# Optimization experiments

Hardware: AMD Instinct MI355X
Metric: run time of the kernel (lower is better)

## Reference

```python
import jax, jax.numpy as jnp
import numpy as np

N_NODES = 20000
N_EDGES = 320000
F_IN, H1, H2, N_CLS = 128, 512, 256, 40
NEG_SLOPE = 0.2


def _glorot(key, shape):
    lim = float(np.sqrt(6.0 / (shape[0] + shape[-1])))
    return jax.random.uniform(key, shape, jnp.float32, -lim, lim)


def setup_inputs() -> dict:
    key = jax.random.key(0)
    ks = jax.random.split(key, 12)
    x = jax.random.normal(ks[0], (N_NODES, F_IN), jnp.float32)
    edge_index = jax.random.randint(ks[1], (2, N_EDGES), 0, N_NODES, jnp.int64)
    params = {}
    dims = [(F_IN, H1), (H1, H2), (H2, N_CLS)]
    for i, (din, dout) in enumerate(dims, start=1):
        params[f"W{i}"] = _glorot(ks[3 * i - 1], (din, dout))
        params[f"a{i}s"] = _glorot(ks[3 * i], (1, dout))[0]
        params[f"a{i}d"] = _glorot(ks[3 * i + 1], (1, dout))[0]
        params[f"b{i}"] = jnp.zeros((dout,), jnp.float32)
    return {"x": x, "edge_index": edge_index, **params}


def gat_conv(x, src, dst, W, a_src, a_dst, b, num_nodes):
    # PyG GATConv, heads=1: h = xW; e_ij = LeakyReLU(a_src.h_j + a_dst.h_i)
    # alpha = softmax over incoming edges of target i; out_i = sum_j alpha_ij h_j + b
    h = x @ W                                        # [N, Dout]
    alpha_s = h @ a_src                              # [N]
    alpha_d = h @ a_dst                              # [N]
    e = jax.nn.leaky_relu(alpha_s[src] + alpha_d[dst], NEG_SLOPE)  # [E]
    m = jax.ops.segment_max(e, dst, num_segments=num_nodes)        # [N]
    ex = jnp.exp(e - m[dst])
    denom = jax.ops.segment_sum(ex, dst, num_segments=num_nodes)   # [N]
    alpha = ex / denom[dst]
    out = jax.ops.segment_sum(alpha[:, None] * h[src], dst, num_segments=num_nodes)
    return out + b


def reference(x, edge_index, W1, a1s, a1d, b1, W2, a2s, a2d, b2, W3, a3s, a3d, b3):
    n = x.shape[0]
    # PyG GATConv adds self-loops by default
    loops = jnp.arange(n, dtype=edge_index.dtype)
    src = jnp.concatenate([edge_index[0], loops])
    dst = jnp.concatenate([edge_index[1], loops])
    h = jax.nn.relu(gat_conv(x, src, dst, W1, a1s, a1d, b1, n))
    h = jax.nn.relu(gat_conv(h, src, dst, W2, a2s, a2d, b2, n))
    h = gat_conv(h, src, dst, W3, a3s, a3d, b3, n)
    return jax.nn.log_softmax(h, axis=1)
```

## Files before the change

### kernel.cpp

```cpp
#include <hip/hip_runtime.h>
#include <math.h>

#define N_NODES 20000
#define N_EDGESC 320000
#define ET (N_EDGESC + N_NODES)
#define F_IN 128
#define H1 512
#define H2 256
#define N_CLS 40
#define NEG_SLOPE 0.2f

typedef __attribute__((ext_vector_type(8))) short short8;
typedef __attribute__((ext_vector_type(4))) float floatx4;

__device__ __forceinline__ unsigned short f2bf(float x) {
    unsigned u = __float_as_uint(x);
    unsigned r = (u + 0x7fffu + ((u >> 16) & 1u)) >> 16;
    return (unsigned short)r;
}
__device__ __forceinline__ float bflo(unsigned v) { return __uint_as_float(v << 16); }
__device__ __forceinline__ float bfhi(unsigned v) { return __uint_as_float(v & 0xffff0000u); }
__device__ __forceinline__ float leaky(float e) { return (e > 0.f) ? e : e * NEG_SLOPE; }

template <int DIN, bool IN_BF16>
__device__ __forceinline__ void gemv2_body(int node, int lane, const void* __restrict__ in,
                                           const float* __restrict__ wvs,
                                           const float* __restrict__ wvd,
                                           float* __restrict__ als, float* __restrict__ ald) {
    constexpr int C = DIN / 64;
    float ss = 0.f, sd = 0.f;
    if constexpr (IN_BF16) {
        const unsigned short* r = (const unsigned short*)in + (size_t)node * DIN + lane * C;
        float f[C];
        if constexpr (C == 8) {
            uint4 v = *(const uint4*)r;
            f[0] = bflo(v.x); f[1] = bfhi(v.x); f[2] = bflo(v.y); f[3] = bfhi(v.y);
            f[4] = bflo(v.z); f[5] = bfhi(v.z); f[6] = bflo(v.w); f[7] = bfhi(v.w);
        } else {
            uint2 v = *(const uint2*)r;
            f[0] = bflo(v.x); f[1] = bfhi(v.x); f[2] = bflo(v.y); f[3] = bfhi(v.y);
        }
        #pragma unroll
        for (int c = 0; c < C; ++c) {
            ss += f[c] * wvs[lane * C + c];
            sd += f[c] * wvd[lane * C + c];
        }
    } else {
        const float* r = (const float*)in + (size_t)node * DIN + lane * 2;
        float2 v = *(const float2*)r;
        ss = v.x * wvs[lane * 2] + v.y * wvs[lane * 2 + 1];
        sd = v.x * wvd[lane * 2] + v.y * wvd[lane * 2 + 1];
    }
    #pragma unroll
    for (int off = 32; off; off >>= 1) {
        ss += __shfl_xor(ss, off);
        sd += __shfl_xor(sd, off);
    }
    if (lane == 0) { als[node] = ss; ald[node] = sd; }
}

#define NCT (F_IN * H1 + H1 * H2 + H2 * N_CLS)
#define PB_CASTX 2500
#define PB_CASTT ((NCT + 255) / 256)
#define PB_WA 224
#define PB_ZERO ((N_NODES + 255) / 256)

__global__ __launch_bounds__(256) void prep_kernel(
        const float* __restrict__ x, unsigned short* __restrict__ xb,
        const float* __restrict__ W1, unsigned short* __restrict__ w1t,
        const float* __restrict__ a1s, const float* __restrict__ a1d,
        const float* __restrict__ W2, unsigned short* __restrict__ w2t,
        const float* __restrict__ a2s, const float* __restrict__ a2d,
        const float* __restrict__ W3, unsigned short* __restrict__ w3t,
        const float* __restrict__ a3s, const float* __restrict__ a3d,
        float* __restrict__ wab, int* __restrict__ deg) {
    int bid = blockIdx.x, t = threadIdx.x;
    if (bid < PB_CASTX) {
        int i = (bid * 256 + t) * 4;
        float4 v = *(const float4*)(x + i);
        ushort4 o = { f2bf(v.x), f2bf(v.y), f2bf(v.z), f2bf(v.w) };
        *(ushort4*)(xb + i) = o;
    } else if (bid < PB_CASTX + PB_CASTT) {
        int i = (bid - PB_CASTX) * 256 + t;
        if (i < F_IN * H1) {
            int k = i >> 9, n = i & 511;
            w1t[n * F_IN + k] = f2bf(W1[i]);
        } else if (i < F_IN * H1 + H1 * H2) {
            int j = i - F_IN * H1;
            int k = j >> 8, n = j & 255;
            w2t[n * H1 + k] = f2bf(W2[j]);
        } else if (i < NCT) {
            int j = i - (F_IN * H1 + H1 * H2);
            int k = j / N_CLS, n = j - k * N_CLS;
            w3t[n * H2 + k] = f2bf(W3[j]);
        }
    } else if (bid < PB_CASTX + PB_CASTT + PB_WA) {
        int lane = t & 63;
        int row = (bid - PB_CASTX - PB_CASTT) * 4 + (t >> 6);
        const float *W, *vs, *vd;
        float *os, *od;
        int N, k;
        if (row < 128)      { k = row;       W = W1; vs = a1s; vd = a1d; os = wab;        od = wab + 128;  N = H1; }
        else if (row < 640) { k = row - 128; W = W2; vs = a2s; vd = a2d; os = wab + 256;  od = wab + 768;  N = H2; }
        else                { k = row - 640; W = W3; vs = a3s; vd = a3d; os = wab + 1280; od = wab + 1536; N = N_CLS; }
        const float* r = W + (size_t)k * N;
        float ss = 0.f, sd = 0.f;
        for (int n = lane; n < N; n += 64) {
            float v = r[n];
            ss += v * vs[n];
            sd += v * vd[n];
        }
        #pragma unroll
        for (int off = 32; off; off >>= 1) {
            ss += __shfl_xor(ss, off);
            sd += __shfl_xor(sd, off);
        }
        if (lane == 0) { os[k] = ss; od[k] = sd; }
    } else {
        int i = (bid - PB_CASTX - PB_CASTT - PB_WA) * 256 + t;
        if (i < N_NODES) deg[i] = 0;
    }
}

#define CB_CNT ((ET + 255) / 256)

__global__ __launch_bounds__(256) void count_gemv1_kernel(
        const int* __restrict__ ei, int* __restrict__ deg,
        const float* __restrict__ x, const float* __restrict__ wab,
        float* __restrict__ als1, float* __restrict__ ald1) {
    int bid = blockIdx.x, t = threadIdx.x;
    if (bid < CB_CNT) {
        int e = bid * 256 + t;
        if (e < ET) {
            int d = (e < N_EDGESC) ? ei[N_EDGESC + e] : (e - N_EDGESC);
            atomicAdd(&deg[d], 1);
        }
    } else {
        int node = (bid - CB_CNT) * 4 + (t >> 6);
        if (node < N_NODES)
            gemv2_body<F_IN, false>(node, t & 63, x, wab, wab + 128, als1, ald1);
    }
}

__global__ __launch_bounds__(1024) void scan_kernel(const int* __restrict__ deg,
                                                    int* __restrict__ rowptr,
                                                    int* __restrict__ writeptr) {
    __shared__ int sums[1024];
    int t = threadIdx.x;
    const int per = (N_NODES + 1023) / 1024;
    int base = t * per;
    int local = 0;
    for (int i = 0; i < per; ++i) {
        int idx = base + i;
        if (idx < N_NODES) local += deg[idx];
    }
    sums[t] = local;
    __syncthreads();
    for (int off = 1; off < 1024; off <<= 1) {
        int add = (t >= off) ? sums[t - off] : 0;
        __syncthreads();
        sums[t] += add;
        __syncthreads();
    }
    int run = sums[t] - local;
    for (int i = 0; i < per; ++i) {
        int idx = base + i;
        if (idx < N_NODES) {
            rowptr[idx] = run;
            writeptr[idx] = run;
            run += deg[idx];
        }
    }
    if (t == 1023) rowptr[N_NODES] = sums[1023];
}

__global__ void fill_kernel(const int* __restrict__ ei, int* __restrict__ writeptr,
                            int* __restrict__ csr_src) {
    int e = blockIdx.x * blockDim.x + threadIdx.x;
    if (e >= ET) return;
    int s, d;
    if (e < N_EDGESC) { s = ei[e]; d = ei[N_EDGESC + e]; }
    else { s = d = e - N_EDGESC; }
    int pos = atomicAdd(&writeptr[d], 1);
    csr_src[pos] = s;
}

#define LDT 40
#define LSO 66

template <int MT, int NT, bool BIASRELU, bool OUT_BF16, int GDIN, bool GBF16>
__global__ __launch_bounds__(256) void gemm_fused(
        const unsigned short* __restrict__ A, const unsigned short* __restrict__ Bt,
        void* __restrict__ Cp, const float* __restrict__ bias,
        int M, int K, int N, int gemm_blocks,
        const void* __restrict__ gin, const float* __restrict__ wvs,
        const float* __restrict__ wvd, float* __restrict__ als, float* __restrict__ ald) {
    constexpr int MI = MT / 64;
    __shared__ unsigned short As[MT * LDT];
    __shared__ unsigned short Bs[64 * LDT];
    __shared__ unsigned short Ls[64 * LSO];
    int bid = blockIdx.x, t = threadIdx.x;
    int w = t >> 6, lane = t & 63;

    if (bid >= gemm_blocks) {
        if constexpr (GDIN > 0) {
            int node = (bid - gemm_blocks) * 4 + w;
            if (node < N_NODES)
                gemv2_body<GDIN, GBF16>(node, lane, gin, wvs, wvd, als, ald);
        }
        return;
    }

    int quad = lane >> 4, l16 = lane & 15;
    int bm = (bid / NT) * MT, bn = (bid % NT) * 64;

    int ar0 = t >> 2;
    int ak = (t & 3) * 8;

    floatx4 acc[MI][4];
    #pragma unroll
    for (int i = 0; i < MI; ++i)
        #pragma unroll
        for (int j = 0; j < 4; ++j) acc[i][j] = (floatx4){0.f, 0.f, 0.f, 0.f};

    uint4 pa0 = {0,0,0,0}, pa1 = {0,0,0,0}, pb = {0,0,0,0};
    {
        int gm0 = bm + ar0, gn = bn + ar0;
        if (gm0 < M) pa0 = *(const uint4*)(A + (size_t)gm0 * K + ak);
        if constexpr (MI == 2) {
            int gm1 = bm + 64 + ar0;
            if (gm1 < M) pa1 = *(const uint4*)(A + (size_t)gm1 * K + ak);
        }
        if (gn < N) pb = *(const uint4*)(Bt + (size_t)gn * K + ak);
    }

    for (int k0 = 0; k0 < K; k0 += 32) {
        *(uint4*)(&As[ar0 * LDT + ak]) = pa0;
        if constexpr (MI == 2) *(uint4*)(&As[(64 + ar0) * LDT + ak]) = pa1;
        *(uint4*)(&Bs[ar0 * LDT + ak]) = pb;
        __syncthreads();

        int kn = k0 + 32;
        if (kn < K) {
            int gm0 = bm + ar0, gn = bn + ar0;
            pa0 = (gm0 < M) ? *(const uint4*)(A + (size_t)gm0 * K + kn + ak) : (uint4){0,0,0,0};
            if constexpr (MI == 2) {
                int gm1 = bm + 64 + ar0;
                pa1 = (gm1 < M) ? *(const uint4*)(A + (size_t)gm1 * K + kn + ak) : (uint4){0,0,0,0};
            }
            pb = (gn < N) ? *(const uint4*)(Bt + (size_t)gn * K + kn + ak) : (uint4){0,0,0,0};
        }

        short8 a[MI], b[4];
        #pragma unroll
        for (int mi = 0; mi < MI; ++mi)
            a[mi] = *(short8*)(&As[(w * (MT / 4) + mi * 16 + l16) * LDT + quad * 8]);
        #pragma unroll
        for (int ni = 0; ni < 4; ++ni)
            b[ni] = *(short8*)(&Bs[(ni * 16 + l16) * LDT + quad * 8]);
        #pragma unroll
        for (int mi = 0; mi < MI; ++mi)
            #pragma unroll
            for (int ni = 0; ni < 4; ++ni)
                acc[mi][ni] = __builtin_amdgcn_mfma_f32_16x16x32_bf16(a[mi], b[ni], acc[mi][ni], 0, 0, 0);
        __syncthreads();
    }

    if constexpr (OUT_BF16) {
        #pragma unroll
        for (int mi = 0; mi < MI; ++mi) {
            #pragma unroll
            for (int ni = 0; ni < 4; ++ni) {
                int col = bn + ni * 16 + l16;
                #pragma unroll
                for (int r = 0; r < 4; ++r) {
                    float v = acc[mi][ni][r];
                    if constexpr (BIASRELU) v = fmaxf(v + bias[col], 0.f);
                    Ls[(w * 16 + quad * 4 + r) * LSO + ni * 16 + l16] = f2bf(v);
                }
            }
            __syncthreads();
            #pragma unroll
            for (int i = 0; i < 2; ++i) {
                int idx = t + i * 256;
                int lrow = idx >> 3, c8 = (idx & 7) * 8;
                int grow = bm + (lrow >> 4) * (MT / 4) + mi * 16 + (lrow & 15);
                if (grow < M)
                    *(uint4*)((unsigned short*)Cp + (size_t)grow * N + bn + c8) =
                        *(uint4*)(&Ls[lrow * LSO + c8]);
            }
            __syncthreads();
        }
    } else {
        #pragma unroll
        for (int mi = 0; mi < MI; ++mi) {
            #pragma unroll
            for (int r = 0; r < 4; ++r) {
                int row = bm + w * (MT / 4) + mi * 16 + quad * 4 + r;
                if (row >= M) continue;
                #pragma unroll
                for (int ni = 0; ni < 4; ++ni) {
                    int col = bn + ni * 16 + l16;
                    if (col < N) ((float*)Cp)[(size_t)row * N + col] = acc[mi][ni][r];
                }
            }
        }
    }
}

template <int DOUT, bool BIAS, bool RELU, bool LSM, bool IN_BF16, bool OUT_BF16>
__global__ __launch_bounds__(256) void agg_kernel(const void* __restrict__ h,
                                                  const float* __restrict__ as,
                                                  const float* __restrict__ ad,
                                                  const int* __restrict__ rowptr,
                                                  const int* __restrict__ csr_src,
                                                  const float* __restrict__ bias,
                                                  void* __restrict__ outp) {
    constexpr int C = (DOUT + 63) / 64;
    int wave = threadIdx.x >> 6, lane = threadIdx.x & 63;
    int node = blockIdx.x * 4 + wave;
    if (node >= N_NODES) return;
    int beg = rowptr[node], end = rowptr[node + 1];
    float adi = ad[node];

    int k0 = beg + lane;
    bool has0 = k0 < end;
    int sj = has0 ? csr_src[k0] : 0;
    float ej = -INFINITY;
    if (has0) ej = leaky(as[sj] + adi);

    float m = ej;
    for (int k = k0 + 64; k < end; k += 64) m = fmaxf(m, leaky(as[csr_src[k]] + adi));
    #pragma unroll
    for (int off = 32; off; off >>= 1) m = fmaxf(m, __shfl_xor(m, off));

    float den = has0 ? expf(ej - m) : 0.f;
    for (int k = k0 + 64; k < end; k += 64) den += expf(leaky(as[csr_src[k]] + adi) - m);
    #pragma unroll
    for (int off = 32; off; off >>= 1) den += __shfl_xor(den, off);
    float invden = 1.f / den;

    float wgt = has0 ? expf(ej - m) * invden : 0.f;

    float acc[C];
    #pragma unroll
    for (int c = 0; c < C; ++c) acc[c] = 0.f;

    auto fetch = [&](int s, float* f) {
        if constexpr (IN_BF16) {
            const unsigned short* hr = (const unsigned short*)h + (size_t)s * DOUT + lane * C;
            if constexpr (C == 8) {
                uint4 v = *(const uint4*)hr;
                f[0] = bflo(v.x); f[1] = bfhi(v.x); f[2] = bflo(v.y); f[3] = bfhi(v.y);
                f[4] = bflo(v.z); f[5] = bfhi(v.z); f[6] = bflo(v.w); f[7] = bfhi(v.w);
            } else if constexpr (C == 4) {
                uint2 v = *(const uint2*)hr;
                f[0] = bflo(v.x); f[1] = bfhi(v.x); f[2] = bflo(v.y); f[3] = bfhi(v.y);
            } else {
                unsigned v = *(const unsigned*)hr;
                f[0] = bflo(v); f[1] = bfhi(v);
            }
        } else {
            if (lane < DOUT) f[0] = ((const float*)h)[(size_t)s * DOUT + lane];
            else f[0] = 0.f;
        }
    };

    int cnt0 = min(64, end - beg);
    int j = 0;
    for (; j + 7 < cnt0; j += 8) {
        int s[8]; float a[8]; float f[8][C];
        #pragma unroll
        for (int u = 0; u < 8; ++u) { s[u] = __shfl(sj, j + u); a[u] = __shfl(wgt, j + u); }
        #pragma unroll
        for (int u = 0; u < 8; ++u) fetch(s[u], f[u]);
        #pragma unroll
        for (int u = 0; u < 8; ++u)
            #pragma unroll
            for (int c = 0; c < C; ++c) acc[c] += a[u] * f[u][c];
    }
    for (; j < cnt0; ++j) {
        int s0 = __shfl(sj, j);
        float a0 = __shfl(wgt, j);
        float f0[C];
        fetch(s0, f0);
        #pragma unroll
        for (int c = 0; c < C; ++c) acc[c] += a0 * f0[c];
    }
    for (int base = beg + 64; base < end; base += 64) {
        int cnt = min(64, end - base);
        int sx = 0; float wx = 0.f;
        if (lane < cnt) {
            sx = csr_src[base + lane];
            wx = expf(leaky(as[sx] + adi) - m) * invden;
        }
        for (int jj = 0; jj < cnt; ++jj) {
            int s0 = __shfl(sx, jj);
            float a0 = __shfl(wx, jj);
            float f0[C];
            fetch(s0, f0);
            #pragma unroll
            for (int c = 0; c < C; ++c) acc[c] += a0 * f0[c];
        }
    }

    if constexpr (!LSM) {
        #pragma unroll
        for (int c = 0; c < C; ++c) {
            int col = lane * C + c;
            if (DOUT % 64 == 0 || col < DOUT) {
                float v = acc[c];
                if constexpr (BIAS) v += bias[col];
                if constexpr (RELU) v = fmaxf(v, 0.f);
                if constexpr (OUT_BF16)
                    ((unsigned short*)outp)[(size_t)node * DOUT + col] = f2bf(v);
                else
                    ((float*)outp)[(size_t)node * DOUT + col] = v;
            }
        }
    } else {
        float v = (lane < DOUT) ? (acc[0] + bias[lane]) : -INFINITY;
        float mm = v;
        #pragma unroll
        for (int off = 32; off; off >>= 1) mm = fmaxf(mm, __shfl_xor(mm, off));
        float ex = (lane < DOUT) ? expf(v - mm) : 0.f;
        float Z = ex;
        #pragma unroll
        for (int off = 32; off; off >>= 1) Z += __shfl_xor(Z, off);
        if (lane < DOUT) ((float*)outp)[(size_t)node * DOUT + lane] = v - mm - logf(Z);
    }
}


extern "C" void kernel_launch(void* const* d_in, const int* in_sizes, int n_in,
                              void* d_out, int out_size, void* d_ws, size_t ws_size,
                              hipStream_t stream) {
    const float* x   = (const float*)d_in[0];
    const int*   ei  = (const int*)d_in[1];
    const float* W1  = (const float*)d_in[2];
    const float* a1s = (const float*)d_in[3];
    const float* a1d = (const float*)d_in[4];
    const float* b1  = (const float*)d_in[5];
    const float* W2  = (const float*)d_in[6];
    const float* a2s = (const float*)d_in[7];
    const float* a2d = (const float*)d_in[8];
    const float* b2  = (const float*)d_in[9];
    const float* W3  = (const float*)d_in[10];
    const float* a3s = (const float*)d_in[11];
    const float* a3d = (const float*)d_in[12];
    const float* b3  = (const float*)d_in[13];
    float* out = (float*)d_out;

    char* ws = (char*)d_ws;
    size_t off = 0;
    auto alloc = [&](size_t bytes) {
        void* p = ws + off;
        off = (off + bytes + 255) & ~(size_t)255;
        return p;
    };
    int*            deg      = (int*)alloc(N_NODES * 4);
    int*            writeptr = (int*)alloc(N_NODES * 4);
    int*            rowptr   = (int*)alloc((N_NODES + 1) * 4);
    int*            csr_src  = (int*)alloc((size_t)ET * 4);
    float*          alph     = (float*)alloc((size_t)6 * N_NODES * 4);
    float*          wab      = (float*)alloc(1792 * 4);
    unsigned short* xb       = (unsigned short*)alloc((size_t)N_NODES * F_IN * 2);
    unsigned short* w1t      = (unsigned short*)alloc((size_t)H1 * F_IN * 2);
    unsigned short* w2t      = (unsigned short*)alloc((size_t)H2 * H1 * 2);
    unsigned short* w3t      = (unsigned short*)alloc((size_t)N_CLS * H2 * 2);
    unsigned short* zb       = (unsigned short*)alloc((size_t)N_NODES * F_IN * 2);
    unsigned short* y1       = (unsigned short*)alloc((size_t)N_NODES * H1 * 2);
    unsigned short* h2       = (unsigned short*)alloc((size_t)N_NODES * H2 * 2);
    float*          h3       = (float*)alloc((size_t)N_NODES * N_CLS * 4);
    (void)alloc(128 * 1024);

    unsigned short* y2 = y1;

    float* als1 = alph + 0 * N_NODES; float* ald1 = alph + 1 * N_NODES;
    float* als2 = alph + 2 * N_NODES; float* ald2 = alph + 3 * N_NODES;
    float* als3 = alph + 4 * N_NODES; float* ald3 = alph + 5 * N_NODES;

    dim3 blk(256);
    int nodeblocks = (N_NODES + 3) / 4;
    const int mt128 = (N_NODES + 127) / 128;
    const int mt64  = (N_NODES + 63) / 64;

    prep_kernel<<<PB_CASTX + PB_CASTT + PB_WA + PB_ZERO, blk, 0, stream>>>(
        x, xb, W1, w1t, a1s, a1d, W2, w2t, a2s, a2d, W3, w3t, a3s, a3d, wab, deg);
    count_gemv1_kernel<<<CB_CNT + nodeblocks, blk, 0, stream>>>(ei, deg, x, wab, als1, ald1);
    scan_kernel<<<1, 1024, 0, stream>>>(deg, rowptr, writeptr);
    fill_kernel<<<(ET + 255) / 256, blk, 0, stream>>>(ei, writeptr, csr_src);

    agg_kernel<F_IN, false, false, false, true, true><<<nodeblocks, blk, 0, stream>>>(
        xb, als1, ald1, rowptr, csr_src, nullptr, zb);
    gemm_fused<128, 8, true, true, 0, false><<<8 * mt128, blk, 0, stream>>>(
        zb, w1t, y1, b1, N_NODES, F_IN, H1, 8 * mt128,
        nullptr, nullptr, nullptr, nullptr, nullptr);
    gemm_fused<128, 4, false, true, H1, true><<<4 * mt128 + nodeblocks, blk, 0, stream>>>(
        y1, w2t, h2, nullptr, N_NODES, H1, H2, 4 * mt128,
        y1, wab + 256, wab + 768, als2, ald2);
    agg_kernel<H2, true, true, false, true, true><<<nodeblocks, blk, 0, stream>>>(
        h2, als2, ald2, rowptr, csr_src, b2, y2);
    gemm_fused<64, 1, false, false, H2, true><<<mt64 + nodeblocks, blk, 0, stream>>>(
        y2, w3t, h3, nullptr, N_NODES, H2, N_CLS, mt64,
        y2, wab + 1280, wab + 1536, als3, ald3);
    agg_kernel<N_CLS, true, false, true, false, false><<<nodeblocks, blk, 0, stream>>>(
        h3, als3, ald3, rowptr, csr_src, b3, out);
}
```

Measured before the change: 262.4 us.

## Replace CSR build with fixed-slot adjacency plus overflow list; fuse layer-3 attention GEMV

Drops the separate scan and fill kernels by writing each edge's source directly into a fixed 64-slot per-node array during the degree-count pass. Edges beyond 64 go to a global overflow list, which aggregation scans linearly. The aggregation kernel for layer 2 now also computes the layer-3 attention projections, so the layer-3 GEMM no longer carries GEMV blocks. This removes two launches and a single-block serial scan. In exchange it uses a larger padded adjacency buffer, caps the overflow list at a fixed size, and makes edge order within each node nondeterministic.

```diff
diff --git a/kernel.cpp b/kernel.cpp
--- a/kernel.cpp
+++ b/kernel.cpp
@@ -9,6 +9,7 @@
 #define H2 256
 #define N_CLS 40
 #define NEG_SLOPE 0.2f
+#define DEGMAX 64
 
 typedef __attribute__((ext_vector_type(8))) short short8;
 typedef __attribute__((ext_vector_type(4))) float floatx4;
@@ -63,7 +64,7 @@
 #define PB_CASTX 2500
 #define PB_CASTT ((NCT + 255) / 256)
 #define PB_WA 224
-#define PB_ZERO ((N_NODES + 255) / 256)
+#define PB_ZERO ((N_NODES + 1 + 255) / 256)
 
 __global__ __launch_bounds__(256) void prep_kernel(
         const float* __restrict__ x, unsigned short* __restrict__ xb,
@@ -73,7 +74,7 @@
         const float* __restrict__ a2s, const float* __restrict__ a2d,
         const float* __restrict__ W3, unsigned short* __restrict__ w3t,
         const float* __restrict__ a3s, const float* __restrict__ a3d,
-        float* __restrict__ wab, int* __restrict__ deg) {
+        float* __restrict__ wab, int* __restrict__ deg, int* __restrict__ ocnt) {
     int bid = blockIdx.x, t = threadIdx.x;
     if (bid < PB_CASTX) {
         int i = (bid * 256 + t) * 4;
@@ -119,21 +120,31 @@
     } else {
         int i = (bid - PB_CASTX - PB_CASTT - PB_WA) * 256 + t;
         if (i < N_NODES) deg[i] = 0;
+        else if (i == N_NODES) *ocnt = 0;
     }
 }
 
 #define CB_CNT ((ET + 255) / 256)
 
-__global__ __launch_bounds__(256) void count_gemv1_kernel(
+__global__ __launch_bounds__(256) void fill_gemv1_kernel(
         const int* __restrict__ ei, int* __restrict__ deg,
+        int* __restrict__ csr_src, int* __restrict__ ocnt, int* __restrict__ oflow,
         const float* __restrict__ x, const float* __restrict__ wab,
         float* __restrict__ als1, float* __restrict__ ald1) {
     int bid = blockIdx.x, t = threadIdx.x;
     if (bid < CB_CNT) {
         int e = bid * 256 + t;
         if (e < ET) {
-            int d = (e < N_EDGESC) ? ei[N_EDGESC + e] : (e - N_EDGESC);
-            atomicAdd(&deg[d], 1);
+            int s, d;
+            if (e < N_EDGESC) { s = ei[e]; d = ei[N_EDGESC + e]; }
+            else { s = d = e - N_EDGESC; }
+            int slot = atomicAdd(&deg[d], 1);
+            if (slot < DEGMAX) csr_src[(d << 6) + slot] = s;
+            else {
+                int o = atomicAdd(ocnt, 1);
+                oflow[2 * o] = d;
+                oflow[2 * o + 1] = s;
+            }
         }
     } else {
         int node = (bid - CB_CNT) * 4 + (t >> 6);
@@ -142,47 +153,146 @@
     }
 }
 
-__global__ __launch_bounds__(1024) void scan_kernel(const int* __restrict__ deg,
-                                                    int* __restrict__ rowptr,
-                                                    int* __restrict__ writeptr) {
-    __shared__ int sums[1024];
-    int t = threadIdx.x;
-    const int per = (N_NODES + 1023) / 1024;
-    int base = t * per;
-    int local = 0;
-    for (int i = 0; i < per; ++i) {
-        int idx = base + i;
-        if (idx < N_NODES) local += deg[idx];
-    }
-    sums[t] = local;
-    __syncthreads();
-    for (int off = 1; off < 1024; off <<= 1) {
-        int add = (t >= off) ? sums[t - off] : 0;
-        __syncthreads();
-        sums[t] += add;
-        __syncthreads();
-    }
-    int run = sums[t] - local;
-    for (int i = 0; i < per; ++i) {
-        int idx = base + i;
-        if (idx < N_NODES) {
-            rowptr[idx] = run;
-            writeptr[idx] = run;
-            run += deg[idx];
-        }
-    }
-    if (t == 1023) rowptr[N_NODES] = sums[1023];
-}
-
-__global__ void fill_kernel(const int* __restrict__ ei, int* __restrict__ writeptr,
-                            int* __restrict__ csr_src) {
-    int e = blockIdx.x * blockDim.x + threadIdx.x;
-    if (e >= ET) return;
-    int s, d;
-    if (e < N_EDGESC) { s = ei[e]; d = ei[N_EDGESC + e]; }
-    else { s = d = e - N_EDGESC; }
-    int pos = atomicAdd(&writeptr[d], 1);
-    csr_src[pos] = s;
+template <int DOUT, bool BIAS, bool RELU, bool LSM, bool IN_BF16, bool OUT_BF16, bool ALPHA3>
+__global__ __launch_bounds__(256) void agg_kernel(const void* __restrict__ h,
+                                                  const float* __restrict__ as,
+                                                  const float* __restrict__ ad,
+                                                  const int* __restrict__ deg,
+                                                  const int* __restrict__ csr_src,
+                                                  const int* __restrict__ ocnt,
+                                                  const int* __restrict__ oflow,
+                                                  const float* __restrict__ bias,
+                                                  void* __restrict__ outp,
+                                                  const float* __restrict__ wv3s,
+                                                  const float* __restrict__ wv3d,
+                                                  float* __restrict__ o3s,
+                                                  float* __restrict__ o3d) {
+    constexpr int C = (DOUT + 63) / 64;
+    int wave = threadIdx.x >> 6, lane = threadIdx.x & 63;
+    int node = blockIdx.x * 4 + wave;
+    if (node >= N_NODES) return;
+    int degt = deg[node];
+    int cnt = min(degt, DEGMAX);
+    int base = node << 6;
+    float adi = ad[node];
+    bool ovf = degt > DEGMAX;
+    int novf = ovf ? *ocnt : 0;
+
+    bool has0 = lane < cnt;
+    int sj = has0 ? csr_src[base + lane] : 0;
+    float ej = has0 ? leaky(as[sj] + adi) : -INFINITY;
+
+    float m = ej;
+    if (ovf) {
+        for (int i = lane; i < novf; i += 64)
+            if (oflow[2 * i] == node) m = fmaxf(m, leaky(as[oflow[2 * i + 1]] + adi));
+    }
+    #pragma unroll
+    for (int off = 32; off; off >>= 1) m = fmaxf(m, __shfl_xor(m, off));
+
+    float den = has0 ? expf(ej - m) : 0.f;
+    if (ovf) {
+        for (int i = lane; i < novf; i += 64)
+            if (oflow[2 * i] == node) den += expf(leaky(as[oflow[2 * i + 1]] + adi) - m);
+    }
+    #pragma unroll
+    for (int off = 32; off; off >>= 1) den += __shfl_xor(den, off);
+    float invden = 1.f / den;
+
+    float wgt = has0 ? expf(ej - m) * invden : 0.f;
+
+    float acc[C];
+    #pragma unroll
+    for (int c = 0; c < C; ++c) acc[c] = 0.f;
+
+    auto fetch = [&](int s, float* f) {
+        if constexpr (IN_BF16) {
+            const unsigned short* hr = (const unsigned short*)h + (size_t)s * DOUT + lane * C;
+            if constexpr (C == 8) {
+                uint4 v = *(const uint4*)hr;
+                f[0] = bflo(v.x); f[1] = bfhi(v.x); f[2] = bflo(v.y); f[3] = bfhi(v.y);
+                f[4] = bflo(v.z); f[5] = bfhi(v.z); f[6] = bflo(v.w); f[7] = bfhi(v.w);
+            } else if constexpr (C == 4) {
+                uint2 v = *(const uint2*)hr;
+                f[0] = bflo(v.x); f[1] = bfhi(v.x); f[2] = bflo(v.y); f[3] = bfhi(v.y);
+            } else {
+                unsigned v = *(const unsigned*)hr;
+                f[0] = bflo(v); f[1] = bfhi(v);
+            }
+        } else {
+            if (lane < DOUT) f[0] = ((const float*)h)[(size_t)s * DOUT + lane];
+            else f[0] = 0.f;
+        }
+    };
+
+    int j = 0;
+    for (; j + 7 < cnt; j += 8) {
+        int s[8]; float a[8]; float f[8][C];
+        #pragma unroll
+        for (int u = 0; u < 8; ++u) { s[u] = __shfl(sj, j + u); a[u] = __shfl(wgt, j + u); }
+        #pragma unroll
+        for (int u = 0; u < 8; ++u) fetch(s[u], f[u]);
+        #pragma unroll
+        for (int u = 0; u < 8; ++u)
+            #pragma unroll
+            for (int c = 0; c < C; ++c) acc[c] += a[u] * f[u][c];
+    }
+    for (; j < cnt; ++j) {
+        int s0 = __shfl(sj, j);
+        float a0 = __shfl(wgt, j);
+        float f0[C];
+        fetch(s0, f0);
+        #pragma unroll
+        for (int c = 0; c < C; ++c) acc[c] += a0 * f0[c];
+    }
+    if (ovf) {
+        for (int i = 0; i < novf; ++i) {
+            if (oflow[2 * i] == node) {
+                int s0 = oflow[2 * i + 1];
+                float a0 = expf(leaky(as[s0] + adi) - m) * invden;
+                float f0[C];
+                fetch(s0, f0);
+                #pragma unroll
+                for (int c = 0; c < C; ++c) acc[c] += a0 * f0[c];
+            }
+        }
+    }
+
+    if constexpr (!LSM) {
+        float ps = 0.f, pd = 0.f;
+        #pragma unroll
+        for (int c = 0; c < C; ++c) {
+            int col = lane * C + c;
+            if (DOUT % 64 == 0 || col < DOUT) {
+                float v = acc[c];
+                if constexpr (BIAS) v += bias[col];
+                if constexpr (RELU) v = fmaxf(v, 0.f);
+                if constexpr (ALPHA3) { ps += v * wv3s[col]; pd += v * wv3d[col]; }
+                if constexpr (OUT_BF16)
+                    ((unsigned short*)outp)[(size_t)node * DOUT + col] = f2bf(v);
+                else
+                    ((float*)outp)[(size_t)node * DOUT + col] = v;
+            }
+        }
+        if constexpr (ALPHA3) {
+            #pragma unroll
+            for (int off = 32; off; off >>= 1) {
+                ps += __shfl_xor(ps, off);
+                pd += __shfl_xor(pd, off);
+            }
+            if (lane == 0) { o3s[node] = ps; o3d[node] = pd; }
+        }
+    } else {
+        float v = (lane < DOUT) ? (acc[0] + bias[lane]) : -INFINITY;
+        float mm = v;
+        #pragma unroll
+        for (int off = 32; off; off >>= 1) mm = fmaxf(mm, __shfl_xor(mm, off));
+        float ex = (lane < DOUT) ? expf(v - mm) : 0.f;
+        float Z = ex;
+        #pragma unroll
+        for (int off = 32; off; off >>= 1) Z += __shfl_xor(Z, off);
+        if (lane < DOUT) ((float*)outp)[(size_t)node * DOUT + lane] = v - mm - logf(Z);
+    }
 }
 
 #define LDT 40
@@ -213,7 +323,6 @@
 
     int quad = lane >> 4, l16 = lane & 15;
     int bm = (bid / NT) * MT, bn = (bid % NT) * 64;
-
     int ar0 = t >> 2;
     int ak = (t & 3) * 8;
 
@@ -305,129 +414,6 @@
                 }
             }
         }
-    }
-}
-
-template <int DOUT, bool BIAS, bool RELU, bool LSM, bool IN_BF16, bool OUT_BF16>
-__global__ __launch_bounds__(256) void agg_kernel(const void* __restrict__ h,
-                                                  const float* __restrict__ as,
-                                                  const float* __restrict__ ad,
-                                                  const int* __restrict__ rowptr,
-                                                  const int* __restrict__ csr_src,
-                                                  const float* __restrict__ bias,
-                                                  void* __restrict__ outp) {
-    constexpr int C = (DOUT + 63) / 64;
-    int wave = threadIdx.x >> 6, lane = threadIdx.x & 63;
-    int node = blockIdx.x * 4 + wave;
-    if (node >= N_NODES) return;
-    int beg = rowptr[node], end = rowptr[node + 1];
-    float adi = ad[node];
-
-    int k0 = beg + lane;
-    bool has0 = k0 < end;
-    int sj = has0 ? csr_src[k0] : 0;
-    float ej = -INFINITY;
-    if (has0) ej = leaky(as[sj] + adi);
-
-    float m = ej;
-    for (int k = k0 + 64; k < end; k += 64) m = fmaxf(m, leaky(as[csr_src[k]] + adi));
-    #pragma unroll
-    for (int off = 32; off; off >>= 1) m = fmaxf(m, __shfl_xor(m, off));
-
-    float den = has0 ? expf(ej - m) : 0.f;
-    for (int k = k0 + 64; k < end; k += 64) den += expf(leaky(as[csr_src[k]] + adi) - m);
-    #pragma unroll
-    for (int off = 32; off; off >>= 1) den += __shfl_xor(den, off);
-    float invden = 1.f / den;
-
-    float wgt = has0 ? expf(ej - m) * invden : 0.f;
-
-    float acc[C];
-    #pragma unroll
-    for (int c = 0; c < C; ++c) acc[c] = 0.f;
-
-    auto fetch = [&](int s, float* f) {
-        if constexpr (IN_BF16) {
-            const unsigned short* hr = (const unsigned short*)h + (size_t)s * DOUT + lane * C;
-            if constexpr (C == 8) {
-                uint4 v = *(const uint4*)hr;
-                f[0] = bflo(v.x); f[1] = bfhi(v.x); f[2] = bflo(v.y); f[3] = bfhi(v.y);
-                f[4] = bflo(v.z); f[5] = bfhi(v.z); f[6] = bflo(v.w); f[7] = bfhi(v.w);
-            } else if constexpr (C == 4) {
-                uint2 v = *(const uint2*)hr;
-                f[0] = bflo(v.x); f[1] = bfhi(v.x); f[2] = bflo(v.y); f[3] = bfhi(v.y);
-            } else {
-                unsigned v = *(const unsigned*)hr;
-                f[0] = bflo(v); f[1] = bfhi(v);
-            }
-        } else {
-            if (lane < DOUT) f[0] = ((const float*)h)[(size_t)s * DOUT + lane];
-            else f[0] = 0.f;
-        }
-    };
-
-    int cnt0 = min(64, end - beg);
-    int j = 0;
-    for (; j + 7 < cnt0; j += 8) {
-        int s[8]; float a[8]; float f[8][C];
-        #pragma unroll
-        for (int u = 0; u < 8; ++u) { s[u] = __shfl(sj, j + u); a[u] = __shfl(wgt, j + u); }
-        #pragma unroll
-        for (int u = 0; u < 8; ++u) fetch(s[u], f[u]);
-        #pragma unroll
-        for (int u = 0; u < 8; ++u)
-            #pragma unroll
-            for (int c = 0; c < C; ++c) acc[c] += a[u] * f[u][c];
-    }
-    for (; j < cnt0; ++j) {
-        int s0 = __shfl(sj, j);
-        float a0 = __shfl(wgt, j);
-        float f0[C];
-        fetch(s0, f0);
-        #pragma unroll
-        for (int c = 0; c < C; ++c) acc[c] += a0 * f0[c];
-    }
-    for (int base = beg + 64; base < end; base += 64) {
-        int cnt = min(64, end - base);
-        int sx = 0; float wx = 0.f;
-        if (lane < cnt) {
-            sx = csr_src[base + lane];
-            wx = expf(leaky(as[sx] + adi) - m) * invden;
-        }
-        for (int jj = 0; jj < cnt; ++jj) {
-            int s0 = __shfl(sx, jj);
-            float a0 = __shfl(wx, jj);
-            float f0[C];
-            fetch(s0, f0);
-            #pragma unroll
-            for (int c = 0; c < C; ++c) acc[c] += a0 * f0[c];
-        }
-    }
-
-    if constexpr (!LSM) {
-        #pragma unroll
-        for (int c = 0; c < C; ++c) {
-            int col = lane * C + c;
-            if (DOUT % 64 == 0 || col < DOUT) {
-                float v = acc[c];
-                if constexpr (BIAS) v += bias[col];
-                if constexpr (RELU) v = fmaxf(v, 0.f);
-                if constexpr (OUT_BF16)
-                    ((unsigned short*)outp)[(size_t)node * DOUT + col] = f2bf(v);
-                else
-                    ((float*)outp)[(size_t)node * DOUT + col] = v;
-            }
-        }
-    } else {
-        float v = (lane < DOUT) ? (acc[0] + bias[lane]) : -INFINITY;
-        float mm = v;
-        #pragma unroll
-        for (int off = 32; off; off >>= 1) mm = fmaxf(mm, __shfl_xor(mm, off));
-        float ex = (lane < DOUT) ? expf(v - mm) : 0.f;
-        float Z = ex;
-        #pragma unroll
-        for (int off = 32; off; off >>= 1) Z += __shfl_xor(Z, off);
-        if (lane < DOUT) ((float*)outp)[(size_t)node * DOUT + lane] = v - mm - logf(Z);
     }
 }
 
@@ -459,9 +445,9 @@
         return p;
     };
     int*            deg      = (int*)alloc(N_NODES * 4);
-    int*            writeptr = (int*)alloc(N_NODES * 4);
-    int*            rowptr   = (int*)alloc((N_NODES + 1) * 4);
-    int*            csr_src  = (int*)alloc((size_t)ET * 4);
+    int*            ocnt     = (int*)alloc(4);
+    int*            oflow    = (int*)alloc(2 * 8192 * 4);
+    int*            csr_src  = (int*)alloc((size_t)N_NODES * DEGMAX * 4);
     float*          alph     = (float*)alloc((size_t)6 * N_NODES * 4);
     float*          wab      = (float*)alloc(1792 * 4);
     unsigned short* xb       = (unsigned short*)alloc((size_t)N_NODES * F_IN * 2);
@@ -486,24 +472,22 @@
     const int mt64  = (N_NODES + 63) / 64;
 
     prep_kernel<<<PB_CASTX + PB_CASTT + PB_WA + PB_ZERO, blk, 0, stream>>>(
-        x, xb, W1, w1t, a1s, a1d, W2, w2t, a2s, a2d, W3, w3t, a3s, a3d, wab, deg);
-    count_gemv1_kernel<<<CB_CNT + nodeblocks, blk, 0, stream>>>(ei, deg, x, wab, als1, ald1);
-    scan_kernel<<<1, 1024, 0, stream>>>(deg, rowptr, writeptr);
-    fill_kernel<<<(ET + 255) / 256, blk, 0, stream>>>(ei, writeptr, csr_src);
-
-    agg_kernel<F_IN, false, false, false, true, true><<<nodeblocks, blk, 0, stream>>>(
-        xb, als1, ald1, rowptr, csr_src, nullptr, zb);
+        x, xb, W1, w1t, a1s, a1d, W2, w2t, a2s, a2d, W3, w3t, a3s, a3d, wab, deg, ocnt);
+    fill_gemv1_kernel<<<CB_CNT + nodeblocks, blk, 0, stream>>>(
+        ei, deg, csr_src, ocnt, oflow, x, wab, als1, ald1);
+    agg_kernel<F_IN, false, false, false, true, true, false><<<nodeblocks, blk, 0, stream>>>(
+        xb, als1, ald1, deg, csr_src, ocnt, oflow, nullptr, zb, nullptr, nullptr, nullptr, nullptr);
     gemm_fused<128, 8, true, true, 0, false><<<8 * mt128, blk, 0, stream>>>(
         zb, w1t, y1, b1, N_NODES, F_IN, H1, 8 * mt128,
         nullptr, nullptr, nullptr, nullptr, nullptr);
     gemm_fused<128, 4, false, true, H1, true><<<4 * mt128 + nodeblocks, blk, 0, stream>>>(
         y1, w2t, h2, nullptr, N_NODES, H1, H2, 4 * mt128,
         y1, wab + 256, wab + 768, als2, ald2);
-    agg_kernel<H2, true, true, false, true, true><<<nodeblocks, blk, 0, stream>>>(
-        h2, als2, ald2, rowptr, csr_src, b2, y2);
-    gemm_fused<64, 1, false, false, H2, true><<<mt64 + nodeblocks, blk, 0, stream>>>(
+    agg_kernel<H2, true, true, false, true, true, true><<<nodeblocks, blk, 0, stream>>>(
+        h2, als2, ald2, deg, csr_src, ocnt, oflow, b2, y2, wab + 1280, wab + 1536, als3, ald3);
+    gemm_fused<64, 1, false, false, 0, false><<<mt64, blk, 0, stream>>>(
         y2, w3t, h3, nullptr, N_NODES, H2, N_CLS, mt64,
-        y2, wab + 1280, wab + 1536, als3, ald3);
-    agg_kernel<N_CLS, true, false, true, false, false><<<nodeblocks, blk, 0, stream>>>(
-        h3, als3, ald3, rowptr, csr_src, b3, out);
-}
+        nullptr, nullptr, nullptr, nullptr, nullptr);
+    agg_kernel<N_CLS, true, false, true, false, false, false><<<nodeblocks, blk, 0, stream>>>(
+        h3, als3, ald3, deg, csr_src, ocnt, oflow, b3, out, nullptr, nullptr, nullptr, nullptr);
+}
```

New measurement: 212.7 us, median of 2. 1.23x faster.
